# Performance work log

Measured on AMD Instinct MI355X. Metric: run time of the kernel, lower is better.

## Reference

```python
import jax, jax.numpy as jnp
import numpy as np
import math

N_HEAD = 16

def setup_inputs() -> dict:
    key = jax.random.key(0)
    k1, k2, k3 = jax.random.split(key, 3)
    B, S, D = 4, 2048, 1024
    x = jax.random.normal(k1, (B, S, D), dtype=jnp.float32)
    w_attn = jax.random.normal(k2, (3 * D, D), dtype=jnp.float32) * 0.02
    b_attn = jnp.zeros((3 * D,), dtype=jnp.float32)
    w_proj = jax.random.normal(k3, (D, D), dtype=jnp.float32) * 0.02
    b_proj = jnp.zeros((D,), dtype=jnp.float32)
    return {"x": x, "w_attn": w_attn, "b_attn": b_attn, "w_proj": w_proj, "b_proj": b_proj}


def reference(x, w_attn, b_attn, w_proj, b_proj):
    B, S, D = x.shape
    H = N_HEAD
    hd = D // H
    # c_attn: nn.Linear -> x @ W^T + b, then split into q,k,v
    qkv = x @ w_attn.T + b_attn                      # [B,S,3D]
    q, k, v = jnp.split(qkv, 3, axis=-1)
    # split heads -> [B,H,S,hd]
    q = q.reshape(B, S, H, hd).transpose(0, 2, 1, 3)
    k = k.reshape(B, S, H, hd).transpose(0, 2, 1, 3)
    v = v.reshape(B, S, H, hd).transpose(0, 2, 1, 3)
    # scaled causal attention (scale=True divides by sqrt(head_dim))
    scores = jnp.einsum('bhqd,bhkd->bhqk', q, k) / math.sqrt(hd)
    mask = jnp.tril(jnp.ones((S, S), dtype=bool))
    scores = jnp.where(mask[None, None], scores, jnp.float32(-1e10))
    w = jax.nn.softmax(scores, axis=-1)
    a = jnp.einsum('bhqk,bhkd->bhqd', w, v)          # [B,H,S,hd]
    # merge heads
    a = a.transpose(0, 2, 1, 3).reshape(B, S, D)
    # c_proj: Conv1D -> x @ W + b with W [nx, nf]
    out = a @ w_proj + b_proj
    # present = stack(key [B,H,S,hd], value [B,H,S,hd])
    present = jnp.stack((k, v))
    return out, present
```

## Files before the change

kernel.cpp:

```cpp
#include <hip/hip_runtime.h>
#include <hip/hip_bf16.h>
#include <stdint.h>

typedef unsigned short u16t;
typedef short s8v __attribute__((ext_vector_type(8)));
typedef float f32x4 __attribute__((ext_vector_type(4)));

#define BB 4
#define SS 2048
#define DD 1024
#define HH 16
#define HD 64
#define MROWS (BB*SS)
#define OUT_ELEMS (MROWS*DD)
#define KV_ELEMS (MROWS*DD)

__device__ __forceinline__ u16t f2bf(float f) {
  union { float f; unsigned int u; } v; v.f = f;
  unsigned int u = v.u;
  unsigned int r = (u + 0x7FFFu + ((u >> 16) & 1u)) >> 16;
  return (u16t)r;
}

__device__ __forceinline__ void async_copy16(u16t* lds_dst, const u16t* g_src) {
  __builtin_amdgcn_global_load_lds(
      (const __attribute__((address_space(1))) unsigned int*)(g_src),
      (__attribute__((address_space(3))) unsigned int*)(lds_dst),
      16, 0, 0);
}

__global__ void convert_f32_bf16(const float* __restrict__ in, u16t* __restrict__ out) {
  int i = (blockIdx.x * blockDim.x + threadIdx.x) * 4;
  float4 f = *(const float4*)(in + i);
  ushort4 o;
  o.x = f2bf(f.x); o.y = f2bf(f.y); o.z = f2bf(f.z); o.w = f2bf(f.w);
  *(ushort4*)(out + i) = o;
}

__global__ void transpose_to_bf16(const float* __restrict__ W, u16t* __restrict__ WT) {
  __shared__ float tile[64][65];
  int bx = blockIdx.x & 15;
  int by = blockIdx.x >> 4;
  int t = threadIdx.x;
  int c = t & 63, r0 = t >> 6;
  for (int i = 0; i < 16; i++) {
    int r = r0 * 16 + i;
    tile[r][c] = W[(size_t)(by*64 + r)*1024 + bx*64 + c];
  }
  __syncthreads();
  for (int i = 0; i < 16; i++) {
    int r = r0 * 16 + i;
    WT[(size_t)(bx*64 + r)*1024 + by*64 + c] = f2bf(tile[c][r]);
  }
}

template<int MODE>
__global__ __launch_bounds__(256)
void gemm_bt(const u16t* __restrict__ A, const u16t* __restrict__ Bm,
             const float* __restrict__ bias, float* __restrict__ outF,
             u16t* __restrict__ qb, u16t* __restrict__ kb, u16t* __restrict__ vb,
             float* __restrict__ presK, float* __restrict__ presV,
             int M, int N, int K) {
  __shared__ u16t As[128*32];
  __shared__ u16t Bs[128*32];
  int tiles_n = N >> 7;
  int bm = blockIdx.x / tiles_n, bn = blockIdx.x % tiles_n;
  int t = threadIdx.x;
  int w = t >> 6, l = t & 63;
  int wm = (w >> 1) * 64, wn = (w & 1) * 64;
  int lr = l & 15, lg = l >> 4;
  int r4 = l >> 2, c8 = (l & 3) * 8;
  const u16t* Ab = A  + (size_t)(bm * 128) * K;
  const u16t* Bb = Bm + (size_t)(bn * 128) * K;

  f32x4 acc[4][4] = {};

  for (int k0 = 0; k0 < K; k0 += 32) {
    __syncthreads();
    async_copy16(As + w*512,        Ab + (size_t)(w*16 + r4)*K      + k0 + c8);
    async_copy16(As + 2048 + w*512, Ab + (size_t)(64 + w*16 + r4)*K + k0 + c8);
    async_copy16(Bs + w*512,        Bb + (size_t)(w*16 + r4)*K      + k0 + c8);
    async_copy16(Bs + 2048 + w*512, Bb + (size_t)(64 + w*16 + r4)*K + k0 + c8);
    __syncthreads();
    s8v a[4], b[4];
#pragma unroll
    for (int mf = 0; mf < 4; mf++) a[mf] = *(s8v*)&As[(wm + mf*16 + lr)*32 + lg*8];
#pragma unroll
    for (int nf = 0; nf < 4; nf++) b[nf] = *(s8v*)&Bs[(wn + nf*16 + lr)*32 + lg*8];
#pragma unroll
    for (int mf = 0; mf < 4; mf++)
#pragma unroll
      for (int nf = 0; nf < 4; nf++)
        acc[mf][nf] = __builtin_amdgcn_mfma_f32_16x16x32_bf16(a[mf], b[nf], acc[mf][nf], 0, 0, 0);
  }

#pragma unroll
  for (int mf = 0; mf < 4; mf++)
#pragma unroll
    for (int nf = 0; nf < 4; nf++)
#pragma unroll
      for (int j = 0; j < 4; j++) {
        int m = bm*128 + wm + mf*16 + lg*4 + j;
        int n = bn*128 + wn + nf*16 + lr;
        float val = acc[mf][nf][j] + bias[n];
        if (MODE == 1) {
          outF[(size_t)m * N + n] = val;
        } else {
          int part = n >> 10, nn = n & 1023;
          int h = nn >> 6, d = nn & 63;
          int bi = m >> 11, s = m & 2047;
          size_t idx = ((size_t)(bi*HH + h)*SS + s)*HD + d;
          if (part == 0) {
            qb[idx] = f2bf(val * 0.125f);
          } else if (part == 1) {
            kb[idx] = f2bf(val); presK[idx] = val;
          } else {
            vb[((size_t)(bi*HH + h)*HD + d)*SS + s] = f2bf(val);
            presV[idx] = val;
          }
        }
      }
}

__global__ __launch_bounds__(256, 3)
void attn_kernel(const u16t* __restrict__ qb, const u16t* __restrict__ kb,
                 const u16t* __restrict__ vtb, u16t* __restrict__ ab) {
  __shared__ u16t Ks[2][64*64];
  __shared__ u16t Vs[2][64*64];
  __shared__ u16t Ps[4*16*72];

  int bid = blockIdx.x;
  int logical = (bid & 7) * 256 + (bid >> 3);
  int bh = logical >> 5;
  int qt = 31 - (logical & 31);
  int q0 = qt * 64;
  int t = threadIdx.x, w = t >> 6, l = t & 63;
  int lr = l & 15, lg = l >> 4;
  const u16t* Qg = qb  + (size_t)bh * SS * HD;
  const u16t* Kg = kb  + (size_t)bh * SS * HD;
  const u16t* Vg = vtb + (size_t)bh * HD * SS;

  int Rrow = t >> 3;
  int csrc = (((((t & 7) >> 1) ^ (Rrow & 3)) << 1) | (t & 1)) * 8;

  s8v qa0 = *(const s8v*)&Qg[(size_t)(q0 + w*16 + lr)*HD + lg*8];
  s8v qa1 = *(const s8v*)&Qg[(size_t)(q0 + w*16 + lr)*HD + 32 + lg*8];

  f32x4 o[4] = {};
  float mrow[4], lrow[4];
#pragma unroll
  for (int j = 0; j < 4; j++) { mrow[j] = -1e30f; lrow[j] = 0.f; }

  u16t* Pw = &Ps[w*16*72];

  auto swz = [](int R, int c) { return R*64 + (((c >> 1) ^ (R & 3)) << 4) + ((c & 1) << 3); };

  int nt = qt + 1;
  {
    int kv0 = 0;
#pragma unroll
    for (int r = 0; r < 2; r++) {
      async_copy16(&Ks[0][(size_t)(r*256 + w*64) * 8], Kg + (size_t)(kv0 + r*32 + Rrow)*HD + csrc);
      async_copy16(&Vs[0][(size_t)(r*256 + w*64) * 8], Vg + (size_t)(r*32 + Rrow)*SS + kv0 + csrc);
    }
  }
  __syncthreads();

  int cur = 0;
  for (int tt = 0; tt < nt; tt++) {
    int kv0 = tt * 64;
    if (tt + 1 < nt) {
      int kn = kv0 + 64;
#pragma unroll
      for (int r = 0; r < 2; r++) {
        async_copy16(&Ks[cur^1][(size_t)(r*256 + w*64) * 8], Kg + (size_t)(kn + r*32 + Rrow)*HD + csrc);
        async_copy16(&Vs[cur^1][(size_t)(r*256 + w*64) * 8], Vg + (size_t)(r*32 + Rrow)*SS + kn + csrc);
      }
    }

    const u16t* Kt = Ks[cur];
    const u16t* Vt = Vs[cur];
    f32x4 s[4];
#pragma unroll
    for (int nf = 0; nf < 4; nf++) {
      int R = nf*16 + lr;
      s8v bk0 = *(const s8v*)&Kt[swz(R, lg)];
      s8v bk1 = *(const s8v*)&Kt[swz(R, 4 + lg)];
      f32x4 a = {};
      a = __builtin_amdgcn_mfma_f32_16x16x32_bf16(qa0, bk0, a, 0, 0, 0);
      a = __builtin_amdgcn_mfma_f32_16x16x32_bf16(qa1, bk1, a, 0, 0, 0);
      s[nf] = a;
    }
    if (tt == qt) {
#pragma unroll
      for (int nf = 0; nf < 4; nf++)
#pragma unroll
        for (int j = 0; j < 4; j++) {
          int row = w*16 + lg*4 + j;
          int col = nf*16 + lr;
          if (col > row) s[nf][j] = -1e30f;
        }
    }
    float resc[4];
#pragma unroll
    for (int j = 0; j < 4; j++) {
      float mx = fmaxf(fmaxf(s[0][j], s[1][j]), fmaxf(s[2][j], s[3][j]));
      mx = fmaxf(mx, __shfl_xor(mx, 1));
      mx = fmaxf(mx, __shfl_xor(mx, 2));
      mx = fmaxf(mx, __shfl_xor(mx, 4));
      mx = fmaxf(mx, __shfl_xor(mx, 8));
      float mnew = fmaxf(mrow[j], mx);
      float sum = 0.f;
#pragma unroll
      for (int nf = 0; nf < 4; nf++) {
        float p = __expf(s[nf][j] - mnew);
        s[nf][j] = p;
        sum += p;
      }
      sum += __shfl_xor(sum, 1);
      sum += __shfl_xor(sum, 2);
      sum += __shfl_xor(sum, 4);
      sum += __shfl_xor(sum, 8);
      float r = __expf(mrow[j] - mnew);
      lrow[j] = lrow[j]*r + sum;
      mrow[j] = mnew;
      resc[j] = r;
    }
#pragma unroll
    for (int nf = 0; nf < 4; nf++)
#pragma unroll
      for (int j = 0; j < 4; j++) o[nf][j] *= resc[j];

#pragma unroll
    for (int nf = 0; nf < 4; nf++)
#pragma unroll
      for (int j = 0; j < 4; j++)
        Pw[(lg*4 + j)*72 + nf*16 + lr] = f2bf(s[nf][j]);
    s8v pa0 = *(s8v*)&Pw[lr*72 + lg*8];
    s8v pa1 = *(s8v*)&Pw[lr*72 + 32 + lg*8];
#pragma unroll
    for (int nf = 0; nf < 4; nf++) {
      int R = nf*16 + lr;
      s8v vv0 = *(const s8v*)&Vt[swz(R, lg)];
      s8v vv1 = *(const s8v*)&Vt[swz(R, 4 + lg)];
      o[nf] = __builtin_amdgcn_mfma_f32_16x16x32_bf16(pa0, vv0, o[nf], 0, 0, 0);
      o[nf] = __builtin_amdgcn_mfma_f32_16x16x32_bf16(pa1, vv1, o[nf], 0, 0, 0);
    }

    __syncthreads();
    cur ^= 1;
  }

  int bi = bh >> 4, h = bh & 15;
#pragma unroll
  for (int nf = 0; nf < 4; nf++)
#pragma unroll
    for (int j = 0; j < 4; j++) {
      int row = q0 + w*16 + lg*4 + j;
      int col = h*HD + nf*16 + lr;
      float val = o[nf][j] / lrow[j];
      ab[((size_t)bi*SS + row)*DD + col] = f2bf(val);
    }
}

extern "C" void kernel_launch(void* const* d_in, const int* in_sizes, int n_in,
                              void* d_out, int out_size, void* d_ws, size_t ws_size,
                              hipStream_t stream) {
  const float* x      = (const float*)d_in[0];
  const float* w_attn = (const float*)d_in[1];
  const float* b_attn = (const float*)d_in[2];
  const float* w_proj = (const float*)d_in[3];
  const float* b_proj = (const float*)d_in[4];
  float* out   = (float*)d_out;
  float* presK = out + (size_t)OUT_ELEMS;
  float* presV = presK + (size_t)KV_ELEMS;

  u16t* ws    = (u16t*)d_ws;
  u16t* x_bf  = ws;
  u16t* wa_bf = x_bf  + (size_t)OUT_ELEMS;
  u16t* wpT   = wa_bf + 3145728;
  u16t* q_bf  = wpT   + 1048576;
  u16t* k_bf  = q_bf  + (size_t)KV_ELEMS;
  u16t* vt_bf = k_bf  + (size_t)KV_ELEMS;
  u16t* a_bf  = x_bf;

  convert_f32_bf16<<<8192, 256, 0, stream>>>(x, x_bf);
  convert_f32_bf16<<<3072, 256, 0, stream>>>(w_attn, wa_bf);
  transpose_to_bf16<<<256, 256, 0, stream>>>(w_proj, wpT);

  gemm_bt<0><<<64*24, 256, 0, stream>>>(x_bf, wa_bf, b_attn, nullptr,
                                        q_bf, k_bf, vt_bf, presK, presV,
                                        MROWS, 3*DD, DD);
  attn_kernel<<<64*32, 256, 0, stream>>>(q_bf, k_bf, vt_bf, a_bf);
  gemm_bt<1><<<64*8, 256, 0, stream>>>(a_bf, wpT, b_proj, out,
                                       nullptr, nullptr, nullptr, nullptr, nullptr,
                                       MROWS, DD, DD);
}
```

Measured before the change: 401.9 us.

## Compute transposed QK^T scores so softmax is per-lane and P moves via shuffles

Swaps the MFMA operand order so each lane holds one query row's scores across keys. The row max and sum then need two cross-lane shuffles instead of four shuffles per row. The P tile is packed to bf16 with v_cvt_pk_bf16_f32 and redistributed with register shuffles rather than a round trip through shared memory. This frees the P shared buffer, and the launch-bounds occupancy hint rises from 3 to 4 blocks, at the cost of extra shuffle and select instructions.

```diff
diff --git a/kernel.cpp b/kernel.cpp
--- a/kernel.cpp
+++ b/kernel.cpp
@@ -122,12 +122,11 @@
       }
 }
 
-__global__ __launch_bounds__(256, 3)
+__global__ __launch_bounds__(256, 4)
 void attn_kernel(const u16t* __restrict__ qb, const u16t* __restrict__ kb,
                  const u16t* __restrict__ vtb, u16t* __restrict__ ab) {
   __shared__ u16t Ks[2][64*64];
   __shared__ u16t Vs[2][64*64];
-  __shared__ u16t Ps[4*16*72];
 
   int bid = blockIdx.x;
   int logical = (bid & 7) * 256 + (bid >> 3);
@@ -147,24 +146,21 @@
   s8v qa1 = *(const s8v*)&Qg[(size_t)(q0 + w*16 + lr)*HD + 32 + lg*8];
 
   f32x4 o[4] = {};
-  float mrow[4], lrow[4];
-#pragma unroll
-  for (int j = 0; j < 4; j++) { mrow[j] = -1e30f; lrow[j] = 0.f; }
-
-  u16t* Pw = &Ps[w*16*72];
+  float m_ = -1e30f, l_ = 0.f;
 
   auto swz = [](int R, int c) { return R*64 + (((c >> 1) ^ (R & 3)) << 4) + ((c & 1) << 3); };
 
   int nt = qt + 1;
-  {
-    int kv0 = 0;
-#pragma unroll
-    for (int r = 0; r < 2; r++) {
-      async_copy16(&Ks[0][(size_t)(r*256 + w*64) * 8], Kg + (size_t)(kv0 + r*32 + Rrow)*HD + csrc);
-      async_copy16(&Vs[0][(size_t)(r*256 + w*64) * 8], Vg + (size_t)(r*32 + Rrow)*SS + kv0 + csrc);
-    }
+#pragma unroll
+  for (int r = 0; r < 2; r++) {
+    async_copy16(&Ks[0][(size_t)(r*256 + w*64) * 8], Kg + (size_t)(r*32 + Rrow)*HD + csrc);
+    async_copy16(&Vs[0][(size_t)(r*256 + w*64) * 8], Vg + (size_t)(r*32 + Rrow)*SS + csrc);
   }
   __syncthreads();
+
+  int src0 = (l & 15) | ((l & 16) << 1);
+  int src1 = src0 + 16;
+  bool hi = (l & 32) != 0;
 
   int cur = 0;
   for (int tt = 0; tt < nt; tt++) {
@@ -180,6 +176,7 @@
 
     const u16t* Kt = Ks[cur];
     const u16t* Vt = Vs[cur];
+
     f32x4 s[4];
 #pragma unroll
     for (int nf = 0; nf < 4; nf++) {
@@ -187,80 +184,102 @@
       s8v bk0 = *(const s8v*)&Kt[swz(R, lg)];
       s8v bk1 = *(const s8v*)&Kt[swz(R, 4 + lg)];
       f32x4 a = {};
-      a = __builtin_amdgcn_mfma_f32_16x16x32_bf16(qa0, bk0, a, 0, 0, 0);
-      a = __builtin_amdgcn_mfma_f32_16x16x32_bf16(qa1, bk1, a, 0, 0, 0);
+      a = __builtin_amdgcn_mfma_f32_16x16x32_bf16(bk0, qa0, a, 0, 0, 0);
+      a = __builtin_amdgcn_mfma_f32_16x16x32_bf16(bk1, qa1, a, 0, 0, 0);
       s[nf] = a;
     }
     if (tt == qt) {
+      int qrow = w*16 + lr;
 #pragma unroll
       for (int nf = 0; nf < 4; nf++)
 #pragma unroll
         for (int j = 0; j < 4; j++) {
-          int row = w*16 + lg*4 + j;
-          int col = nf*16 + lr;
-          if (col > row) s[nf][j] = -1e30f;
+          int kv = nf*16 + lg*4 + j;
+          if (kv > qrow) s[nf][j] = -1e30f;
         }
     }
-    float resc[4];
-#pragma unroll
-    for (int j = 0; j < 4; j++) {
-      float mx = fmaxf(fmaxf(s[0][j], s[1][j]), fmaxf(s[2][j], s[3][j]));
-      mx = fmaxf(mx, __shfl_xor(mx, 1));
-      mx = fmaxf(mx, __shfl_xor(mx, 2));
-      mx = fmaxf(mx, __shfl_xor(mx, 4));
-      mx = fmaxf(mx, __shfl_xor(mx, 8));
-      float mnew = fmaxf(mrow[j], mx);
-      float sum = 0.f;
-#pragma unroll
-      for (int nf = 0; nf < 4; nf++) {
+
+    float pmax = s[0][0];
+#pragma unroll
+    for (int nf = 0; nf < 4; nf++)
+#pragma unroll
+      for (int j = 0; j < 4; j++) pmax = fmaxf(pmax, s[nf][j]);
+    pmax = fmaxf(pmax, __shfl_xor(pmax, 16));
+    pmax = fmaxf(pmax, __shfl_xor(pmax, 32));
+    float mnew = fmaxf(m_, pmax);
+    float psum = 0.f;
+#pragma unroll
+    for (int nf = 0; nf < 4; nf++)
+#pragma unroll
+      for (int j = 0; j < 4; j++) {
         float p = __expf(s[nf][j] - mnew);
         s[nf][j] = p;
-        sum += p;
+        psum += p;
       }
-      sum += __shfl_xor(sum, 1);
-      sum += __shfl_xor(sum, 2);
-      sum += __shfl_xor(sum, 4);
-      sum += __shfl_xor(sum, 8);
-      float r = __expf(mrow[j] - mnew);
-      lrow[j] = lrow[j]*r + sum;
-      mrow[j] = mnew;
-      resc[j] = r;
-    }
-#pragma unroll
-    for (int nf = 0; nf < 4; nf++)
-#pragma unroll
-      for (int j = 0; j < 4; j++) o[nf][j] *= resc[j];
-
-#pragma unroll
-    for (int nf = 0; nf < 4; nf++)
-#pragma unroll
-      for (int j = 0; j < 4; j++)
-        Pw[(lg*4 + j)*72 + nf*16 + lr] = f2bf(s[nf][j]);
-    s8v pa0 = *(s8v*)&Pw[lr*72 + lg*8];
-    s8v pa1 = *(s8v*)&Pw[lr*72 + 32 + lg*8];
+    psum += __shfl_xor(psum, 16);
+    psum += __shfl_xor(psum, 32);
+    float r_ = __expf(m_ - mnew);
+    l_ = l_ * r_ + psum;
+    m_ = mnew;
+
+    float r0f = __shfl(r_, 4*lg + 0);
+    float r1f = __shfl(r_, 4*lg + 1);
+    float r2f = __shfl(r_, 4*lg + 2);
+    float r3f = __shfl(r_, 4*lg + 3);
+#pragma unroll
+    for (int nf = 0; nf < 4; nf++) {
+      o[nf][0] *= r0f; o[nf][1] *= r1f; o[nf][2] *= r2f; o[nf][3] *= r3f;
+    }
+
+    uint32_t s01[4], s23[4];
+#pragma unroll
+    for (int nf = 0; nf < 4; nf++) {
+      asm("v_cvt_pk_bf16_f32 %0, %1, %2" : "=v"(s01[nf]) : "v"(s[nf][0]), "v"(s[nf][1]));
+      asm("v_cvt_pk_bf16_f32 %0, %1, %2" : "=v"(s23[nf]) : "v"(s[nf][2]), "v"(s[nf][3]));
+    }
+    union PU { s8v v; uint32_t w[4]; } pa0, pa1;
+    {
+      uint32_t t00 = __shfl(s01[0], src0), t01 = __shfl(s01[1], src0);
+      uint32_t t10 = __shfl(s23[0], src0), t11 = __shfl(s23[1], src0);
+      uint32_t t20 = __shfl(s01[0], src1), t21 = __shfl(s01[1], src1);
+      uint32_t t30 = __shfl(s23[0], src1), t31 = __shfl(s23[1], src1);
+      pa0.w[0] = hi ? t01 : t00; pa0.w[1] = hi ? t11 : t10;
+      pa0.w[2] = hi ? t21 : t20; pa0.w[3] = hi ? t31 : t30;
+      uint32_t u00 = __shfl(s01[2], src0), u01 = __shfl(s01[3], src0);
+      uint32_t u10 = __shfl(s23[2], src0), u11 = __shfl(s23[3], src0);
+      uint32_t u20 = __shfl(s01[2], src1), u21 = __shfl(s01[3], src1);
+      uint32_t u30 = __shfl(s23[2], src1), u31 = __shfl(s23[3], src1);
+      pa1.w[0] = hi ? u01 : u00; pa1.w[1] = hi ? u11 : u10;
+      pa1.w[2] = hi ? u21 : u20; pa1.w[3] = hi ? u31 : u30;
+    }
+
 #pragma unroll
     for (int nf = 0; nf < 4; nf++) {
       int R = nf*16 + lr;
       s8v vv0 = *(const s8v*)&Vt[swz(R, lg)];
       s8v vv1 = *(const s8v*)&Vt[swz(R, 4 + lg)];
-      o[nf] = __builtin_amdgcn_mfma_f32_16x16x32_bf16(pa0, vv0, o[nf], 0, 0, 0);
-      o[nf] = __builtin_amdgcn_mfma_f32_16x16x32_bf16(pa1, vv1, o[nf], 0, 0, 0);
+      o[nf] = __builtin_amdgcn_mfma_f32_16x16x32_bf16(pa0.v, vv0, o[nf], 0, 0, 0);
+      o[nf] = __builtin_amdgcn_mfma_f32_16x16x32_bf16(pa1.v, vv1, o[nf], 0, 0, 0);
     }
 
     __syncthreads();
     cur ^= 1;
   }
 
+  float li0 = 1.f / __shfl(l_, 4*lg + 0);
+  float li1 = 1.f / __shfl(l_, 4*lg + 1);
+  float li2 = 1.f / __shfl(l_, 4*lg + 2);
+  float li3 = 1.f / __shfl(l_, 4*lg + 3);
   int bi = bh >> 4, h = bh & 15;
 #pragma unroll
-  for (int nf = 0; nf < 4; nf++)
-#pragma unroll
-    for (int j = 0; j < 4; j++) {
-      int row = q0 + w*16 + lg*4 + j;
-      int col = h*HD + nf*16 + lr;
-      float val = o[nf][j] / lrow[j];
-      ab[((size_t)bi*SS + row)*DD + col] = f2bf(val);
-    }
+  for (int nf = 0; nf < 4; nf++) {
+    int row = q0 + w*16 + lg*4;
+    int col = h*HD + nf*16 + lr;
+    ab[((size_t)bi*SS + row + 0)*DD + col] = f2bf(o[nf][0] * li0);
+    ab[((size_t)bi*SS + row + 1)*DD + col] = f2bf(o[nf][1] * li1);
+    ab[((size_t)bi*SS + row + 2)*DD + col] = f2bf(o[nf][2] * li2);
+    ab[((size_t)bi*SS + row + 3)*DD + col] = f2bf(o[nf][3] * li3);
+  }
 }
 
 extern "C" void kernel_launch(void* const* d_in, const int* in_sizes, int n_in,
```

After: 369.2 us. 8.1% less time.
